# Performance work log

Measured on AMD Instinct MI355X. Metric: run time of the kernel, lower is better.

Reference implementation:

```python
import jax, jax.numpy as jnp
import numpy as np

PI = float(np.pi)
EPS = 1e-8

N, M, K, D = 20000, 20000, 32, 64
HID, OUT = 64, 192
PPF_OUT = OUT // 3  # 64


def safe_atan2(y, x):
    x_safe = jnp.where(jnp.abs(x) < EPS, jnp.sign(x) * EPS, x)
    return jnp.arctan2(y, x_safe)


def _angle(a, b):
    # a, b: [N, K, 3] -> normalized angle in [0,1]: atan2(|a x b|, a.b)/pi
    y = jnp.sum(a * b, axis=-1, keepdims=True)
    x = jnp.cross(a, b, axis=-1)
    x_norm = jnp.linalg.norm(x, axis=-1, keepdims=True)
    return safe_atan2(x_norm, y) / PI


def calc_ppf(points, point_normals, neighbor_points, neighbor_normals):
    # points [N,3], point_normals [N,3], neighbor_* [N,K,3]
    p = points[:, None, :]
    pn = jnp.broadcast_to(point_normals[:, None, :], neighbor_points.shape)
    vec_d = neighbor_points - p
    d = jnp.linalg.norm(vec_d, axis=-1, keepdims=True)
    angle1 = _angle(pn, vec_d)
    angle2 = _angle(neighbor_normals, vec_d)
    angle3 = _angle(pn, neighbor_normals)
    return jnp.concatenate([d, angle1, angle2, angle3], axis=-1)  # [N,K,4]


def setup_inputs() -> dict:
    key = jax.random.key(0)
    ks = jax.random.split(key, 16)
    inp = {
        "q_pts": jax.random.normal(ks[0], (N, 3), jnp.float32),
        "s_pts": jax.random.normal(ks[1], (M, 3), jnp.float32),
        "s_feats": jax.random.normal(ks[2], (M, D, 3), jnp.float32),
        "neighbor_indices": jax.random.randint(ks[3], (N, K), 0, M, jnp.int32),
        "normals": jax.random.normal(ks[4], (M, 3), jnp.float32),
        # ppf_encoder: Linear(4,HID) -> ReLU -> Linear(HID,HID) -> ReLU -> Linear(HID,PPF_OUT)
        "W1": jax.random.normal(ks[5], (HID, 4), jnp.float32) * 0.5,
        "b1": jnp.zeros((HID,), jnp.float32),
        "W2": jax.random.normal(ks[6], (HID, HID), jnp.float32) * 0.125,
        "b2": jnp.zeros((HID,), jnp.float32),
        "W3": jax.random.normal(ks[7], (PPF_OUT, HID), jnp.float32) * 0.125,
        "b3": jnp.zeros((PPF_OUT,), jnp.float32),
        # gate_proj: Linear(PPF_OUT, OUT)
        "Wg": jax.random.normal(ks[8], (OUT, PPF_OUT), jnp.float32) * 0.125,
        "bg": jnp.zeros((OUT,), jnp.float32),
        # vn_value: VNLinear(D, OUT) -> weight [OUT, D], no bias
        "Wv": jax.random.normal(ks[9], (OUT, D), jnp.float32) * 0.125,
    }
    return inp


def reference(q_pts, s_pts, s_feats, neighbor_indices, normals,
              W1, b1, W2, b2, W3, b3, Wg, bg, Wv):
    # gather neighbors
    neighbor_pts = s_pts[neighbor_indices]        # [N,K,3]
    neighbor_norms = normals[neighbor_indices]    # [N,K,3]
    q_normals = normals[neighbor_indices[:, 0]]   # [N,3]

    ppf = calc_ppf(q_pts, q_normals, neighbor_pts, neighbor_norms)  # [N,K,4]

    h = jax.nn.relu(ppf @ W1.T + b1)
    h = jax.nn.relu(h @ W2.T + b2)
    ppf_encoded = h @ W3.T + b3                   # [N,K,PPF_OUT]
    ppf_mod = jnp.mean(ppf_encoded, axis=1)       # [N,PPF_OUT]
    gate = jax.nn.sigmoid(ppf_mod @ Wg.T + bg)    # [N,OUT]

    neighbor_feats = s_feats[neighbor_indices]    # [N,K,D,3]
    aggregated = jnp.mean(neighbor_feats, axis=1) # [N,D,3]
    transformed = jnp.einsum('od,ndt->not', Wv, aggregated)  # [N,OUT,3]

    return transformed * gate[:, :, None]
```

## Files before the change

kernel.cpp:

```cpp
#include <hip/hip_runtime.h>
#include <math.h>

#define NPTS 20000
#define KNB  32
#define DDIM 64
#define HIDN 64
#define OUTC 192
#define PPB  4

#define WS_W2 0
#define WS_W3 4096
#define WS_W1 8192
#define WS_WG 10240
#define WS_WV 22528
#define WS_FEATS 34816
#define WS_NEED  (69632 + (size_t)NPTS*192*2)

typedef short bf16x8 __attribute__((ext_vector_type(8)));
typedef float f32x4  __attribute__((ext_vector_type(4)));

union BF8 { bf16x8 v; unsigned short us[8]; unsigned u[4]; };

__device__ __forceinline__ unsigned short f2bf(float f) {
  unsigned u = __builtin_bit_cast(unsigned, f);
  u += 0x7fffu + ((u >> 16) & 1u);
  return (unsigned short)(u >> 16);
}
__device__ __forceinline__ float bfhi2f(unsigned hi) {
  return __builtin_bit_cast(float, hi);
}

__device__ __forceinline__ float fast_atan2pi(float y, float x) {
  const float ax = fabsf(x);
  const float mx = fmaxf(fmaxf(ax, y), 1e-30f);
  const float mn = fminf(ax, y);
  const float t  = mn * __builtin_amdgcn_rcpf(mx);
  const float s  = t * t;
  float p = -0.0117212f;
  p = fmaf(p, s,  0.05265332f);
  p = fmaf(p, s, -0.11643287f);
  p = fmaf(p, s,  0.19354346f);
  p = fmaf(p, s, -0.33262347f);
  p = fmaf(p, s,  0.99997726f);
  float r = p * t;
  if (y > ax)  r = 1.5707963268f - r;
  if (x < 0.f) r = 3.1415926536f - r;
  return r * 0.3183098862f;
}

__device__ __forceinline__ float angle3f(float ax, float ay, float az,
                                         float bx, float by, float bz) {
  const float y  = ax*bx + ay*by + az*bz;
  const float cx = ay*bz - az*by;
  const float cy = az*bx - ax*bz;
  const float cz = ax*by - ay*bx;
  const float xn = __builtin_amdgcn_sqrtf(cx*cx + cy*cy + cz*cz);
  return fast_atan2pi(xn, y);
}

__global__ void prep_weights(const float* __restrict__ W1, const float* __restrict__ W2,
                             const float* __restrict__ W3, const float* __restrict__ Wg,
                             const float* __restrict__ Wv, unsigned short* __restrict__ ws)
{
  const int f  = blockIdx.x;
  const int L  = threadIdx.x;
  const int ln = L & 15, lq = L >> 4;
  unsigned short vals[8];
  if (f >= 16 && f < 20) {
    const int ct = f - 16;
#pragma unroll
    for (int j = 0; j < 8; ++j) {
      const float v = (lq == 0 && j < 4) ? W1[(ln + 16*ct)*4 + j] : 0.f;
      vals[j] = f2bf(v);
    }
  } else {
    const float* M; int q;
    if (f < 8)       { M = W2; q = f; }
    else if (f < 16) { M = W3; q = f - 8; }
    else if (f < 44) { M = Wg; q = f - 20; }
    else             { M = Wv; q = f - 44; }
    const int ct = q >> 1, ks = q & 1;
    const float* src = M + (ln + 16*ct)*64 + lq*8 + 32*ks;
#pragma unroll
    for (int j = 0; j < 8; ++j) vals[j] = f2bf(src[j]);
  }
  uint4 w;
  w.x = vals[0] | ((unsigned)vals[1] << 16);
  w.y = vals[2] | ((unsigned)vals[3] << 16);
  w.z = vals[4] | ((unsigned)vals[5] << 16);
  w.w = vals[6] | ((unsigned)vals[7] << 16);
  *(uint4*)&ws[f*512 + L*8] = w;
}

__global__ __launch_bounds__(256) void prep_feats(const float* __restrict__ sf,
                                                  unsigned short* __restrict__ dst) {
  const int i = (blockIdx.x * 256 + threadIdx.x) * 8;
  const float4 x = *(const float4*)&sf[i];
  const float4 y = *(const float4*)&sf[i + 4];
  uint4 w;
  w.x = f2bf(x.x) | ((unsigned)f2bf(x.y) << 16);
  w.y = f2bf(x.z) | ((unsigned)f2bf(x.w) << 16);
  w.z = f2bf(y.x) | ((unsigned)f2bf(y.y) << 16);
  w.w = f2bf(y.z) | ((unsigned)f2bf(y.w) << 16);
  *(uint4*)&dst[i] = w;
}

template<bool BF>
__global__ __launch_bounds__(256, 6)
void ppf_fused(const float* __restrict__ q_pts,
               const float* __restrict__ s_pts,
               const float* __restrict__ s_feats,
               const int*   __restrict__ nbr,
               const float* __restrict__ normals,
               const float* __restrict__ b1, const float* __restrict__ b2,
               const float* __restrict__ b3, const float* __restrict__ bg,
               const unsigned short* __restrict__ wsu,
               float* __restrict__ out)
{
  __shared__ __align__(16) unsigned short s_h[PPB][KNB][72];
  __shared__ __align__(16) unsigned short s_modb[16][72];
  __shared__ __align__(16) unsigned short s_aggb[16][72];
  __shared__ float s_gate[PPB][200];
  float* s_out = (float*)&s_h[0][0][0];

  const int tid  = threadIdx.x;
  const int g    = tid >> 6;
  const int lane = tid & 63;
  const int lq   = lane >> 4;
  const int ln   = lane & 15;
  const int pu   = __builtin_amdgcn_readfirstlane(blockIdx.x * PPB + g);

  {
    const float qx = q_pts[pu*3+0], qy = q_pts[pu*3+1], qz = q_pts[pu*3+2];
    const int   i0 = nbr[pu*KNB];
    const float qnx = normals[i0*3+0], qny = normals[i0*3+1], qnz = normals[i0*3+2];
    const int k  = lane & 31;
    const int mi = nbr[pu*KNB + k];
    const float px = s_pts[mi*3+0], py = s_pts[mi*3+1], pz = s_pts[mi*3+2];
    const float nx = normals[mi*3+0], ny = normals[mi*3+1], nz = normals[mi*3+2];
    const float vx = px - qx, vy = py - qy, vz = pz - qz;
    float* ppfrow = (float*)&s_h[g][k][64];
    if (lane < KNB) {
      ppfrow[1] = angle3f(qnx,qny,qnz, vx,vy,vz);
      ppfrow[2] = angle3f(nx,ny,nz,    vx,vy,vz);
    } else {
      ppfrow[0] = __builtin_amdgcn_sqrtf(vx*vx + vy*vy + vz*vz);
      ppfrow[3] = angle3f(qnx,qny,qnz, nx,ny,nz);
    }
  }

  {
    BF8 a1f[2];
    a1f[0].u[0]=a1f[0].u[1]=a1f[0].u[2]=a1f[0].u[3]=0;
    a1f[1] = a1f[0];
    if (lq == 0) {
#pragma unroll
      for (int rt = 0; rt < 2; ++rt) {
        const float4 pv = *(const float4*)&s_h[g][ln + 16*rt][64];
        a1f[rt].us[0]=f2bf(pv.x); a1f[rt].us[1]=f2bf(pv.y);
        a1f[rt].us[2]=f2bf(pv.z); a1f[rt].us[3]=f2bf(pv.w);
      }
    }
#pragma unroll
    for (int ct = 0; ct < 4; ++ct) {
      const bf16x8 bw = *(const bf16x8*)&wsu[WS_W1 + ct*512 + lane*8];
      const float  bv = b1[ln + 16*ct];
#pragma unroll
      for (int rt = 0; rt < 2; ++rt) {
        f32x4 c = {bv, bv, bv, bv};
        c = __builtin_amdgcn_mfma_f32_16x16x32_bf16(a1f[rt].v, bw, c, 0, 0, 0);
#pragma unroll
        for (int r = 0; r < 4; ++r)
          s_h[g][lq*4 + r + 16*rt][ln + 16*ct] = f2bf(fmaxf(c[r], 0.f));
      }
    }
  }

  {
    bf16x8 wf[8];
#pragma unroll
    for (int fIdx = 0; fIdx < 8; ++fIdx)
      wf[fIdx] = *(const bf16x8*)&wsu[WS_W2 + fIdx*512 + lane*8];
    bf16x8 af[4];
#pragma unroll
    for (int rt = 0; rt < 2; ++rt)
#pragma unroll
      for (int ks = 0; ks < 2; ++ks)
        af[rt*2+ks] = *(const bf16x8*)&s_h[g][ln + 16*rt][lq*8 + ks*32];
#pragma unroll
    for (int ct = 0; ct < 4; ++ct) {
      const float bv = b2[ln + 16*ct];
#pragma unroll
      for (int rt = 0; rt < 2; ++rt) {
        f32x4 c = {bv, bv, bv, bv};
        c = __builtin_amdgcn_mfma_f32_16x16x32_bf16(af[rt*2+0], wf[ct*2+0], c, 0, 0, 0);
        c = __builtin_amdgcn_mfma_f32_16x16x32_bf16(af[rt*2+1], wf[ct*2+1], c, 0, 0, 0);
#pragma unroll
        for (int r = 0; r < 4; ++r)
          s_h[g][lq*4 + r + 16*rt][ln + 16*ct] = f2bf(fmaxf(c[r], 0.f));
      }
    }
  }

  {
    bf16x8 wf[8];
#pragma unroll
    for (int fIdx = 0; fIdx < 8; ++fIdx)
      wf[fIdx] = *(const bf16x8*)&wsu[WS_W3 + fIdx*512 + lane*8];
    bf16x8 af[4];
#pragma unroll
    for (int rt = 0; rt < 2; ++rt)
#pragma unroll
      for (int ks = 0; ks < 2; ++ks)
        af[rt*2+ks] = *(const bf16x8*)&s_h[g][ln + 16*rt][lq*8 + ks*32];
#pragma unroll
    for (int ct = 0; ct < 4; ++ct) {
      const float bv = b3[ln + 16*ct];
      f32x4 c0 = {bv, bv, bv, bv};
      c0 = __builtin_amdgcn_mfma_f32_16x16x32_bf16(af[0], wf[ct*2+0], c0, 0, 0, 0);
      c0 = __builtin_amdgcn_mfma_f32_16x16x32_bf16(af[1], wf[ct*2+1], c0, 0, 0, 0);
      f32x4 c1 = {bv, bv, bv, bv};
      c1 = __builtin_amdgcn_mfma_f32_16x16x32_bf16(af[2], wf[ct*2+0], c1, 0, 0, 0);
      c1 = __builtin_amdgcn_mfma_f32_16x16x32_bf16(af[3], wf[ct*2+1], c1, 0, 0, 0);
      float s = (c0[0]+c0[1]+c0[2]+c0[3]) + (c1[0]+c1[1]+c1[2]+c1[3]);
      s += __shfl_xor(s, 16);
      s += __shfl_xor(s, 32);
      if (lq == 0) s_modb[g][ln + 16*ct] = f2bf(s * (1.f/KNB));
    }
  }

  if constexpr (BF) {
    if (lane < 48) {
      float a0 = 0.f, a1 = 0.f, a2 = 0.f, a3 = 0.f;
      const unsigned short* fb = wsu + WS_FEATS;
      const int co = lane * 4;
#pragma unroll 8
      for (int k = 0; k < KNB; ++k) {
        const int mi = nbr[pu*KNB + k];
        const uint2 v = *(const uint2*)&fb[(size_t)mi*192 + co];
        a0 += bfhi2f(v.x << 16); a1 += bfhi2f(v.x & 0xffff0000u);
        a2 += bfhi2f(v.y << 16); a3 += bfhi2f(v.y & 0xffff0000u);
      }
      const float av0 = a0 * (1.f/KNB), av1 = a1 * (1.f/KNB);
      const float av2 = a2 * (1.f/KNB), av3 = a3 * (1.f/KNB);
      const int e = 4*lane;
      s_aggb[g*3 + ((e+0) % 3)][(e+0)/3] = f2bf(av0);
      s_aggb[g*3 + ((e+1) % 3)][(e+1)/3] = f2bf(av1);
      s_aggb[g*3 + ((e+2) % 3)][(e+2)/3] = f2bf(av2);
      s_aggb[g*3 + ((e+3) % 3)][(e+3)/3] = f2bf(av3);
    }
  } else {
    float s0 = 0.f, s1 = 0.f, s2 = 0.f;
    const int lofs = lane * 3;
#pragma unroll 8
    for (int k = 0; k < KNB; ++k) {
      const int mi = nbr[pu*KNB + k];
      const float* fr = s_feats + (size_t)mi*(DDIM*3) + lofs;
      s0 += fr[0]; s1 += fr[1]; s2 += fr[2];
    }
    s_aggb[g*3+0][lane] = f2bf(s0 * (1.f/KNB));
    s_aggb[g*3+1][lane] = f2bf(s1 * (1.f/KNB));
    s_aggb[g*3+2][lane] = f2bf(s2 * (1.f/KNB));
  }

  __syncthreads();

  {
    const bf16x8 am0 = *(const bf16x8*)&s_modb[ln][lq*8];
    const bf16x8 am1 = *(const bf16x8*)&s_modb[ln][lq*8 + 32];
#pragma unroll
    for (int t = 0; t < 3; ++t) {
      const int ot = g*3 + t;
      const bf16x8 bg0 = *(const bf16x8*)&wsu[WS_WG + (ot*2+0)*512 + lane*8];
      const bf16x8 bg1 = *(const bf16x8*)&wsu[WS_WG + (ot*2+1)*512 + lane*8];
      const float  bv  = bg[ln + 16*ot];
      f32x4 c = {bv, bv, bv, bv};
      c = __builtin_amdgcn_mfma_f32_16x16x32_bf16(am0, bg0, c, 0, 0, 0);
      c = __builtin_amdgcn_mfma_f32_16x16x32_bf16(am1, bg1, c, 0, 0, 0);
      if (lq == 0) {
#pragma unroll
        for (int r = 0; r < 4; ++r)
          s_gate[r][ln + 16*ot] = 1.f / (1.f + __expf(-c[r]));
      }
    }
  }

  {
    const bf16x8 ab0 = *(const bf16x8*)&s_aggb[ln][lq*8];
    const bf16x8 ab1 = *(const bf16x8*)&s_aggb[ln][lq*8 + 32];
    const int gi = ln / 3;
    const int tt = ln - gi*3;
#pragma unroll
    for (int t2 = 0; t2 < 3; ++t2) {
      const int ot = g*3 + t2;
      const bf16x8 av0 = *(const bf16x8*)&wsu[WS_WV + (ot*2+0)*512 + lane*8];
      const bf16x8 av1 = *(const bf16x8*)&wsu[WS_WV + (ot*2+1)*512 + lane*8];
      f32x4 c = {0.f, 0.f, 0.f, 0.f};
      c = __builtin_amdgcn_mfma_f32_16x16x32_bf16(av0, ab0, c, 0, 0, 0);
      c = __builtin_amdgcn_mfma_f32_16x16x32_bf16(av1, ab1, c, 0, 0, 0);
      if (ln < 12) {
#pragma unroll
        for (int r = 0; r < 4; ++r) {
          const int o = 16*ot + lq*4 + r;
          s_out[gi*592 + o*3 + tt] = c[r] * s_gate[gi][o];
        }
      }
    }
  }
  __syncthreads();

  {
    float4* outv = (float4*)out;
    const float4* sov = (const float4*)s_out;
#pragma unroll
    for (int i = 0; i < 3; ++i) {
      const int idx = tid + 256*i;
      if (idx < 576) {
        const int gg  = idx / 144;
        const int off = idx - gg*144;
        outv[(size_t)blockIdx.x * 576 + idx] = sov[gg*148 + off];
      }
    }
  }
}

extern "C" void kernel_launch(void* const* d_in, const int* in_sizes, int n_in,
                              void* d_out, int out_size, void* d_ws, size_t ws_size,
                              hipStream_t stream) {
  const float* q_pts   = (const float*)d_in[0];
  const float* s_pts   = (const float*)d_in[1];
  const float* s_feats = (const float*)d_in[2];
  const int*   nbr     = (const int*)  d_in[3];
  const float* normals = (const float*)d_in[4];
  const float* W1 = (const float*)d_in[5];
  const float* b1 = (const float*)d_in[6];
  const float* W2 = (const float*)d_in[7];
  const float* b2 = (const float*)d_in[8];
  const float* W3 = (const float*)d_in[9];
  const float* b3 = (const float*)d_in[10];
  const float* Wg = (const float*)d_in[11];
  const float* bg = (const float*)d_in[12];
  const float* Wv = (const float*)d_in[13];
  float* out = (float*)d_out;
  unsigned short* ws = (unsigned short*)d_ws;

  hipLaunchKernelGGL(prep_weights, dim3(68), dim3(64), 0, stream,
                     W1, W2, W3, Wg, Wv, ws);
  if (ws_size >= WS_NEED) {
    hipLaunchKernelGGL(prep_feats, dim3(1875), dim3(256), 0, stream,
                       s_feats, ws + WS_FEATS);
    hipLaunchKernelGGL(ppf_fused<true>, dim3(NPTS / PPB), dim3(256), 0, stream,
                       q_pts, s_pts, s_feats, nbr, normals,
                       b1, b2, b3, bg, ws, out);
  } else {
    hipLaunchKernelGGL(ppf_fused<false>, dim3(NPTS / PPB), dim3(256), 0, stream,
                       q_pts, s_pts, s_feats, nbr, normals,
                       b1, b2, b3, bg, ws, out);
  }
}
```

Measured before the change: 159.0 us.

## Merge prep kernels and transpose MFMA operands for packed hidden-layer stores

```diff
diff --git a/kernel.cpp b/kernel.cpp
--- a/kernel.cpp
+++ b/kernel.cpp
@@ -1,4 +1,5 @@
 #include <hip/hip_runtime.h>
+#include <hip/hip_bf16.h>
 #include <math.h>
 
 #define NPTS 20000
@@ -28,6 +29,12 @@
 }
 __device__ __forceinline__ float bfhi2f(unsigned hi) {
   return __builtin_bit_cast(float, hi);
+}
+__device__ __forceinline__ unsigned pack2bf(float lo, float hi) {
+  const __hip_bfloat162 h = __float22bfloat162_rn(make_float2(lo, hi));
+  unsigned u;
+  __builtin_memcpy(&u, &h, 4);
+  return u;
 }
 
 __device__ __forceinline__ float fast_atan2pi(float y, float x) {
@@ -58,11 +65,28 @@
   return fast_atan2pi(xn, y);
 }
 
-__global__ void prep_weights(const float* __restrict__ W1, const float* __restrict__ W2,
-                             const float* __restrict__ W3, const float* __restrict__ Wg,
-                             const float* __restrict__ Wv, unsigned short* __restrict__ ws)
+__global__ __launch_bounds__(256)
+void prep_all(const float* __restrict__ sf,
+              const float* __restrict__ W1, const float* __restrict__ W2,
+              const float* __restrict__ W3, const float* __restrict__ Wg,
+              const float* __restrict__ Wv, unsigned short* __restrict__ ws,
+              int do_feats)
 {
-  const int f  = blockIdx.x;
+  const int b = blockIdx.x;
+  if (b >= 68) {
+    const int i = ((b - 68) * 256 + threadIdx.x) * 8;
+    const float4 x = *(const float4*)&sf[i];
+    const float4 y = *(const float4*)&sf[i + 4];
+    uint4 w;
+    w.x = f2bf(x.x) | ((unsigned)f2bf(x.y) << 16);
+    w.y = f2bf(x.z) | ((unsigned)f2bf(x.w) << 16);
+    w.z = f2bf(y.x) | ((unsigned)f2bf(y.y) << 16);
+    w.w = f2bf(y.z) | ((unsigned)f2bf(y.w) << 16);
+    *(uint4*)&ws[WS_FEATS + i] = w;
+    return;
+  }
+  if (threadIdx.x >= 64) return;
+  const int f  = b;
   const int L  = threadIdx.x;
   const int ln = L & 15, lq = L >> 4;
   unsigned short vals[8];
@@ -90,19 +114,7 @@
   w.z = vals[4] | ((unsigned)vals[5] << 16);
   w.w = vals[6] | ((unsigned)vals[7] << 16);
   *(uint4*)&ws[f*512 + L*8] = w;
-}
-
-__global__ __launch_bounds__(256) void prep_feats(const float* __restrict__ sf,
-                                                  unsigned short* __restrict__ dst) {
-  const int i = (blockIdx.x * 256 + threadIdx.x) * 8;
-  const float4 x = *(const float4*)&sf[i];
-  const float4 y = *(const float4*)&sf[i + 4];
-  uint4 w;
-  w.x = f2bf(x.x) | ((unsigned)f2bf(x.y) << 16);
-  w.y = f2bf(x.z) | ((unsigned)f2bf(x.w) << 16);
-  w.z = f2bf(y.x) | ((unsigned)f2bf(y.y) << 16);
-  w.w = f2bf(y.z) | ((unsigned)f2bf(y.w) << 16);
-  *(uint4*)&dst[i] = w;
+  (void)do_feats;
 }
 
 template<bool BF>
@@ -150,28 +162,29 @@
   }
 
   {
-    BF8 a1f[2];
-    a1f[0].u[0]=a1f[0].u[1]=a1f[0].u[2]=a1f[0].u[3]=0;
-    a1f[1] = a1f[0];
+    BF8 pf[2];
+    pf[0].u[0]=pf[0].u[1]=pf[0].u[2]=pf[0].u[3]=0;
+    pf[1] = pf[0];
     if (lq == 0) {
 #pragma unroll
       for (int rt = 0; rt < 2; ++rt) {
         const float4 pv = *(const float4*)&s_h[g][ln + 16*rt][64];
-        a1f[rt].us[0]=f2bf(pv.x); a1f[rt].us[1]=f2bf(pv.y);
-        a1f[rt].us[2]=f2bf(pv.z); a1f[rt].us[3]=f2bf(pv.w);
+        pf[rt].us[0]=f2bf(pv.x); pf[rt].us[1]=f2bf(pv.y);
+        pf[rt].us[2]=f2bf(pv.z); pf[rt].us[3]=f2bf(pv.w);
       }
     }
 #pragma unroll
     for (int ct = 0; ct < 4; ++ct) {
-      const bf16x8 bw = *(const bf16x8*)&wsu[WS_W1 + ct*512 + lane*8];
-      const float  bv = b1[ln + 16*ct];
+      const bf16x8 aw  = *(const bf16x8*)&wsu[WS_W1 + ct*512 + lane*8];
+      const float4 bv4 = *(const float4*)&b1[ct*16 + lq*4];
 #pragma unroll
       for (int rt = 0; rt < 2; ++rt) {
-        f32x4 c = {bv, bv, bv, bv};
-        c = __builtin_amdgcn_mfma_f32_16x16x32_bf16(a1f[rt].v, bw, c, 0, 0, 0);
-#pragma unroll
-        for (int r = 0; r < 4; ++r)
-          s_h[g][lq*4 + r + 16*rt][ln + 16*ct] = f2bf(fmaxf(c[r], 0.f));
+        f32x4 c = {bv4.x, bv4.y, bv4.z, bv4.w};
+        c = __builtin_amdgcn_mfma_f32_16x16x32_bf16(aw, pf[rt].v, c, 0, 0, 0);
+        uint2 pk;
+        pk.x = pack2bf(fmaxf(c[0], 0.f), fmaxf(c[1], 0.f));
+        pk.y = pack2bf(fmaxf(c[2], 0.f), fmaxf(c[3], 0.f));
+        *(uint2*)&s_h[g][ln + 16*rt][ct*16 + lq*4] = pk;
       }
     }
   }
@@ -181,23 +194,24 @@
 #pragma unroll
     for (int fIdx = 0; fIdx < 8; ++fIdx)
       wf[fIdx] = *(const bf16x8*)&wsu[WS_W2 + fIdx*512 + lane*8];
-    bf16x8 af[4];
+    bf16x8 hf[4];
 #pragma unroll
     for (int rt = 0; rt < 2; ++rt)
 #pragma unroll
       for (int ks = 0; ks < 2; ++ks)
-        af[rt*2+ks] = *(const bf16x8*)&s_h[g][ln + 16*rt][lq*8 + ks*32];
+        hf[rt*2+ks] = *(const bf16x8*)&s_h[g][ln + 16*rt][lq*8 + ks*32];
 #pragma unroll
     for (int ct = 0; ct < 4; ++ct) {
-      const float bv = b2[ln + 16*ct];
+      const float4 bv4 = *(const float4*)&b2[ct*16 + lq*4];
 #pragma unroll
       for (int rt = 0; rt < 2; ++rt) {
-        f32x4 c = {bv, bv, bv, bv};
-        c = __builtin_amdgcn_mfma_f32_16x16x32_bf16(af[rt*2+0], wf[ct*2+0], c, 0, 0, 0);
-        c = __builtin_amdgcn_mfma_f32_16x16x32_bf16(af[rt*2+1], wf[ct*2+1], c, 0, 0, 0);
-#pragma unroll
-        for (int r = 0; r < 4; ++r)
-          s_h[g][lq*4 + r + 16*rt][ln + 16*ct] = f2bf(fmaxf(c[r], 0.f));
+        f32x4 c = {bv4.x, bv4.y, bv4.z, bv4.w};
+        c = __builtin_amdgcn_mfma_f32_16x16x32_bf16(wf[ct*2+0], hf[rt*2+0], c, 0, 0, 0);
+        c = __builtin_amdgcn_mfma_f32_16x16x32_bf16(wf[ct*2+1], hf[rt*2+1], c, 0, 0, 0);
+        uint2 pk;
+        pk.x = pack2bf(fmaxf(c[0], 0.f), fmaxf(c[1], 0.f));
+        pk.y = pack2bf(fmaxf(c[2], 0.f), fmaxf(c[3], 0.f));
+        *(uint2*)&s_h[g][ln + 16*rt][ct*16 + lq*4] = pk;
       }
     }
   }
@@ -344,11 +358,11 @@
   float* out = (float*)d_out;
   unsigned short* ws = (unsigned short*)d_ws;
 
-  hipLaunchKernelGGL(prep_weights, dim3(68), dim3(64), 0, stream,
-                     W1, W2, W3, Wg, Wv, ws);
-  if (ws_size >= WS_NEED) {
-    hipLaunchKernelGGL(prep_feats, dim3(1875), dim3(256), 0, stream,
-                       s_feats, ws + WS_FEATS);
+  const int do_feats = (ws_size >= WS_NEED) ? 1 : 0;
+  const int prep_blocks = do_feats ? (68 + 1875) : 68;
+  hipLaunchKernelGGL(prep_all, dim3(prep_blocks), dim3(256), 0, stream,
+                     s_feats, W1, W2, W3, Wg, Wv, ws, do_feats);
+  if (do_feats) {
     hipLaunchKernelGGL(ppf_fused<true>, dim3(NPTS / PPB), dim3(256), 0, stream,
                        q_pts, s_pts, s_feats, nbr, normals,
                        b1, b2, b3, bg, ws, out);
```

Measured after the change: 158.5 us. About the same (-0.3%).
